# Optimization experiments

Measured on AMD Instinct MI355X. Metric: run time of the kernel, lower is better.

The kernel has to match this reference:

```python
import jax, jax.numpy as jnp
import numpy as np
from jax import lax


def setup_inputs() -> dict:
    key = jax.random.key(0)
    B, H, W, C, L = 16, 256, 256, 3, 8  # L == max_scale level sets
    x = jax.random.uniform(key, (B, H, W, C, L), dtype=jnp.float32)
    return {"x": x, "max_scale": 8}


def reference(x, max_scale):
    # x: [B, H, W, C, L] with L == max_scale
    B, H, W, C, L = x.shape
    # Fuse all level sets into the channel dim so each scale is ONE pooling op
    xr = x.reshape(B, H, W, C * L)
    neg_inf = jnp.asarray(-jnp.inf, dtype=x.dtype)
    per_scale = []
    for scale in range(1, max_scale + 1):
        # MaxPooling2D(pool_size=(scale,scale), strides=(1,1), padding='valid')
        pooled = lax.reduce_window(
            xr, neg_inf, lax.max,
            window_dimensions=(1, scale, scale, 1),
            window_strides=(1, 1, 1, 1),
            padding='VALID',
        )  # [B, H-scale+1, W-scale+1, C*L]
        # reduce_sum over spatial axes -> [B, C*L] -> [B, C, L]
        per_scale.append(pooled.sum(axis=(1, 2)).reshape(B, C, L))
    membership = jnp.stack(per_scale, axis=-1)  # [B, C, L, S]
    return jax.nn.relu(membership) + 1.0
```

## Files before the change

### kernel.cpp

```cpp
#include <hip/hip_runtime.h>
#include <math.h>


namespace {
constexpr int Bn = 16, Hn = 256, Wn = 256, CHn = 24, Sn = 8;
constexpr int IT = 16;
constexpr int NBANDS = Hn / IT;
constexpr int NSTRIP = 32;
constexpr int BDIM = CHn * NSTRIP;
constexpr int ROWF = Wn * CHn;
constexpr int LROW = 6560;
constexpr int OUT_N = Bn * CHn * Sn;
}

__device__ __forceinline__ int lds_addr(int c, int ch) {
  return c * 25 + ch + (c >> 3) * 5;
}

__global__ __launch_bounds__(BDIM, 3) void sgb_main(const float* __restrict__ x,
                                                    float* __restrict__ accum) {
  __shared__ float buf[2][LROW];

  const int band = blockIdx.x;
  const int b    = blockIdx.y;
  const int i0   = band * IT;
  const int tid  = threadIdx.x;
  const int ch    = tid >> 5;
  const int strip = tid & 31;
  const int rbase = strip * 205 + ch;
  const int wbase = lds_addr(tid / 3, (tid % 3) * 8);

  float P[7][8];
#pragma unroll
  for (int s = 0; s < 7; ++s)
#pragma unroll
    for (int j = 0; j < 8; ++j) P[s][j] = -INFINITY;

  float acc[Sn];
#pragma unroll
  for (int s = 0; s < Sn; ++s) acc[s] = 0.f;

  const float* img = x + (long)(b * Hn) * ROWF;
  const int rhi = i0 + IT + 6;

  if (rhi < Hn) {
    const float* src = img + rhi * ROWF + tid * 8;
    float4 v0 = reinterpret_cast<const float4*>(src)[0];
    float4 v1 = reinterpret_cast<const float4*>(src)[1];
    float* d = &buf[0][wbase];
    d[0] = v0.x; d[1] = v0.y; d[2] = v0.z; d[3] = v0.w;
    d[4] = v1.x; d[5] = v1.y; d[6] = v1.z; d[7] = v1.w;
  }

  for (int idx = 0; idx < IT + 7; ++idx) {
    const int r  = rhi - idx;
    const int pb = idx & 1;
    __syncthreads();

    const bool do_stage = (idx < IT + 6) && (r - 1 < Hn);
    float4 v0, v1;
    if (do_stage) {
      const float* src = img + (r - 1) * ROWF + tid * 8;
      v0 = reinterpret_cast<const float4*>(src)[0];
      v1 = reinterpret_cast<const float4*>(src)[1];
    }

    float cp[8];
    if (r < Hn) {
      const float* rb = &buf[pb][rbase];
#pragma unroll
      for (int k = 0; k < 8; ++k) cp[k] = rb[25 * k];
    } else {
#pragma unroll
      for (int k = 0; k < 8; ++k) cp[k] = -INFINITY;
    }

    const bool outrow = (r < i0 + IT);
    if (outrow) {
      acc[0] += ((cp[0] + cp[1]) + (cp[2] + cp[3])) +
                ((cp[4] + cp[5]) + (cp[6] + cp[7]));
    }

#pragma unroll
    for (int s = 2; s <= Sn; ++s) {
      float nbNew = __shfl_down(cp[0], 1);
      float nbOld = __shfl_down(P[s - 2][0], 1);
      float cc[8];
#pragma unroll
      for (int j = 0; j < 7; ++j)
        cc[j] = fmaxf(fmaxf(cp[j], cp[j + 1]),
                      fmaxf(P[s - 2][j], P[s - 2][j + 1]));
      cc[7] = fmaxf(fmaxf(cp[7], nbNew), fmaxf(P[s - 2][7], nbOld));

      if (outrow && (r + s <= Hn)) {
        float lo = 0.f, hi = 0.f;
#pragma unroll
        for (int j = 0; j < 8; ++j) {
          if (j <= 8 - s) lo += cc[j]; else hi += cc[j];
        }
        acc[s - 1] += lo + (strip == NSTRIP - 1 ? 0.f : hi);
      }
#pragma unroll
      for (int j = 0; j < 8; ++j) { P[s - 2][j] = cp[j]; cp[j] = cc[j]; }
    }

    if (do_stage) {
      float* d = &buf[pb ^ 1][wbase];
      d[0] = v0.x; d[1] = v0.y; d[2] = v0.z; d[3] = v0.w;
      d[4] = v1.x; d[5] = v1.y; d[6] = v1.z; d[7] = v1.w;
    }
  }

#pragma unroll
  for (int s = 0; s < Sn; ++s) {
    float v = acc[s];
    v += __shfl_xor(v, 16);
    v += __shfl_xor(v, 8);
    v += __shfl_xor(v, 4);
    v += __shfl_xor(v, 2);
    v += __shfl_xor(v, 1);
    if (strip == 0) atomicAdd(&accum[(b * CHn + ch) * Sn + s], v);
  }
}

__global__ void sgb_finalize(float* __restrict__ out) {
  const int i = blockIdx.x * blockDim.x + threadIdx.x;
  if (i < OUT_N) out[i] = fmaxf(out[i], 0.f) + 1.f;
}

extern "C" void kernel_launch(void* const* d_in, const int* in_sizes, int n_in,
                              void* d_out, int out_size, void* d_ws, size_t ws_size,
                              hipStream_t stream) {
  (void)in_sizes; (void)n_in; (void)d_ws; (void)ws_size; (void)out_size;
  const float* x = (const float*)d_in[0];
  float* out = (float*)d_out;

  hipMemsetAsync(out, 0, OUT_N * sizeof(float), stream);
  dim3 grid(NBANDS, Bn);
  sgb_main<<<grid, BDIM, 0, stream>>>(x, out);
  sgb_finalize<<<(OUT_N + 255) / 256, 256, 0, stream>>>(out);
}
```

Before: 163.7 us.

## Pre-transpose input to channel-planar bf16 and drop LDS staging in main kernel

Adds a transpose kernel that converts the interleaved fp32 input into per-channel bf16 planes in the workspace. The main kernel then streams rows straight from global memory with a register prefetch, removing the shared-memory double buffering and the per-row block barriers, and launches three channel groups per band. This adds an extra full pass of global writes and reads. Reducing inputs to bf16 also loses precision in the large sums.

```diff
diff --git a/kernel.cpp b/kernel.cpp
--- a/kernel.cpp
+++ b/kernel.cpp
@@ -4,31 +4,57 @@
 
 namespace {
 constexpr int Bn = 16, Hn = 256, Wn = 256, CHn = 24, Sn = 8;
-constexpr int IT = 16;
-constexpr int NBANDS = Hn / IT;
-constexpr int NSTRIP = 32;
-constexpr int BDIM = CHn * NSTRIP;
 constexpr int ROWF = Wn * CHn;
 constexpr int LROW = 6560;
+constexpr int TBD  = 768;
+constexpr int IT = 16, NBANDS = Hn / IT;
+constexpr int CHG = 3;
+constexpr int MBD = 256;
+constexpr long PLANE = (long)Hn * Wn;
 constexpr int OUT_N = Bn * CHn * Sn;
 }
 
-__device__ __forceinline__ int lds_addr(int c, int ch) {
-  return c * 25 + ch + (c >> 3) * 5;
+
+__device__ __forceinline__ unsigned bf16pack2(float a, float b) {
+  unsigned ua = __float_as_uint(a), ub = __float_as_uint(b);
+  ua = (ua + 0x7FFFu + ((ua >> 16) & 1u)) >> 16;
+  ub = (ub + 0x7FFFu + ((ub >> 16) & 1u)) & 0xFFFF0000u;
+  return ua | ub;
 }
 
-__global__ __launch_bounds__(BDIM, 3) void sgb_main(const float* __restrict__ x,
-                                                    float* __restrict__ accum) {
-  __shared__ float buf[2][LROW];
+__global__ __launch_bounds__(TBD) void sgb_transpose(const float* __restrict__ x,
+                                                     unsigned short* __restrict__ t) {
+  __shared__ float row[LROW];
+  const int r = blockIdx.x, b = blockIdx.y;
+  const int tid = threadIdx.x;
 
-  const int band = blockIdx.x;
-  const int b    = blockIdx.y;
-  const int i0   = band * IT;
-  const int tid  = threadIdx.x;
-  const int ch    = tid >> 5;
-  const int strip = tid & 31;
-  const int rbase = strip * 205 + ch;
-  const int wbase = lds_addr(tid / 3, (tid % 3) * 8);
+  const float* src = x + ((long)(b * Hn + r)) * ROWF + tid * 8;
+  const float4 v0 = reinterpret_cast<const float4*>(src)[0];
+  const float4 v1 = reinterpret_cast<const float4*>(src)[1];
+  const int wc = tid / 3;
+  float* d = &row[wc * 25 + (tid % 3) * 8 + (wc >> 3) * 5];
+  d[0] = v0.x; d[1] = v0.y; d[2] = v0.z; d[3] = v0.w;
+  d[4] = v1.x; d[5] = v1.y; d[6] = v1.z; d[7] = v1.w;
+  __syncthreads();
+
+  const int ch = tid >> 5, strip = tid & 31;
+  const float* rb = &row[strip * 205 + ch];
+  uint4 o;
+  o.x = bf16pack2(rb[0],   rb[25]);
+  o.y = bf16pack2(rb[50],  rb[75]);
+  o.z = bf16pack2(rb[100], rb[125]);
+  o.w = bf16pack2(rb[150], rb[175]);
+  reinterpret_cast<uint4*>(t + ((long)(b * CHn + ch) * Hn + r) * Wn + strip * 8)[0] = o;
+}
+
+__global__ __launch_bounds__(MBD) void sgb_main(const unsigned short* __restrict__ t,
+                                                float* __restrict__ accum) {
+  const int band = blockIdx.x, cg = blockIdx.y, b = blockIdx.z;
+  const int i0  = band * IT;
+  const int tid = threadIdx.x;
+  const int chl = tid >> 5, strip = tid & 31;
+  const int ch  = cg * 8 + chl;
+  const unsigned short* plane = t + (long)(b * CHn + ch) * PLANE + strip * 8;
 
   float P[7][8];
 #pragma unroll
@@ -40,36 +66,28 @@
 #pragma unroll
   for (int s = 0; s < Sn; ++s) acc[s] = 0.f;
 
-  const float* img = x + (long)(b * Hn) * ROWF;
   const int rhi = i0 + IT + 6;
-
-  if (rhi < Hn) {
-    const float* src = img + rhi * ROWF + tid * 8;
-    float4 v0 = reinterpret_cast<const float4*>(src)[0];
-    float4 v1 = reinterpret_cast<const float4*>(src)[1];
-    float* d = &buf[0][wbase];
-    d[0] = v0.x; d[1] = v0.y; d[2] = v0.z; d[3] = v0.w;
-    d[4] = v1.x; d[5] = v1.y; d[6] = v1.z; d[7] = v1.w;
-  }
+  bool havn = (rhi < Hn);
+  uint4 nxt = make_uint4(0, 0, 0, 0);
+  if (havn) nxt = reinterpret_cast<const uint4*>(plane + (long)rhi * Wn)[0];
 
   for (int idx = 0; idx < IT + 7; ++idx) {
-    const int r  = rhi - idx;
-    const int pb = idx & 1;
-    __syncthreads();
-
-    const bool do_stage = (idx < IT + 6) && (r - 1 < Hn);
-    float4 v0, v1;
-    if (do_stage) {
-      const float* src = img + (r - 1) * ROWF + tid * 8;
-      v0 = reinterpret_cast<const float4*>(src)[0];
-      v1 = reinterpret_cast<const float4*>(src)[1];
-    }
+    const int r = rhi - idx;
+    const uint4 cur = nxt;
+    const bool havc = havn;
+    havn = (idx < IT + 6) && (r - 1 < Hn);
+    if (havn) nxt = reinterpret_cast<const uint4*>(plane + (long)(r - 1) * Wn)[0];
 
     float cp[8];
-    if (r < Hn) {
-      const float* rb = &buf[pb][rbase];
-#pragma unroll
-      for (int k = 0; k < 8; ++k) cp[k] = rb[25 * k];
+    if (havc) {
+      cp[0] = __uint_as_float(cur.x << 16);
+      cp[1] = __uint_as_float(cur.x & 0xFFFF0000u);
+      cp[2] = __uint_as_float(cur.y << 16);
+      cp[3] = __uint_as_float(cur.y & 0xFFFF0000u);
+      cp[4] = __uint_as_float(cur.z << 16);
+      cp[5] = __uint_as_float(cur.z & 0xFFFF0000u);
+      cp[6] = __uint_as_float(cur.w << 16);
+      cp[7] = __uint_as_float(cur.w & 0xFFFF0000u);
     } else {
 #pragma unroll
       for (int k = 0; k < 8; ++k) cp[k] = -INFINITY;
@@ -83,8 +101,8 @@
 
 #pragma unroll
     for (int s = 2; s <= Sn; ++s) {
-      float nbNew = __shfl_down(cp[0], 1);
-      float nbOld = __shfl_down(P[s - 2][0], 1);
+      const float nbNew = __shfl_down(cp[0], 1);
+      const float nbOld = __shfl_down(P[s - 2][0], 1);
       float cc[8];
 #pragma unroll
       for (int j = 0; j < 7; ++j)
@@ -98,16 +116,10 @@
         for (int j = 0; j < 8; ++j) {
           if (j <= 8 - s) lo += cc[j]; else hi += cc[j];
         }
-        acc[s - 1] += lo + (strip == NSTRIP - 1 ? 0.f : hi);
+        acc[s - 1] += lo + (strip == 31 ? 0.f : hi);
       }
 #pragma unroll
       for (int j = 0; j < 8; ++j) { P[s - 2][j] = cp[j]; cp[j] = cc[j]; }
-    }
-
-    if (do_stage) {
-      float* d = &buf[pb ^ 1][wbase];
-      d[0] = v0.x; d[1] = v0.y; d[2] = v0.z; d[3] = v0.w;
-      d[4] = v1.x; d[5] = v1.y; d[6] = v1.z; d[7] = v1.w;
     }
   }
 
@@ -131,12 +143,15 @@
 extern "C" void kernel_launch(void* const* d_in, const int* in_sizes, int n_in,
                               void* d_out, int out_size, void* d_ws, size_t ws_size,
                               hipStream_t stream) {
-  (void)in_sizes; (void)n_in; (void)d_ws; (void)ws_size; (void)out_size;
+  (void)in_sizes; (void)n_in; (void)ws_size; (void)out_size;
   const float* x = (const float*)d_in[0];
   float* out = (float*)d_out;
+  unsigned short* t = (unsigned short*)d_ws;
 
   hipMemsetAsync(out, 0, OUT_N * sizeof(float), stream);
-  dim3 grid(NBANDS, Bn);
-  sgb_main<<<grid, BDIM, 0, stream>>>(x, out);
+  dim3 tg(Hn, Bn);
+  sgb_transpose<<<tg, TBD, 0, stream>>>(x, t);
+  dim3 mg(NBANDS, CHG, Bn);
+  sgb_main<<<mg, MBD, 0, stream>>>(t, out);
   sgb_finalize<<<(OUT_N + 255) / 256, 256, 0, stream>>>(out);
 }
```

Result: slower. 189.4 us (+15.7%).

## Split channels across blocks and stage rows in LDS as packed bf16

Applied to the files above, without the earlier changes.

Adds a channel-group grid dimension so each 256-thread block handles 8 of the 24 channels, and raises launch bounds to target more resident blocks. Staged rows are converted to bf16 pairs in a padded LDS layout, halving shared-memory footprint and read traffic. The rotated neighbour value is cached in registers instead of being re-shuffled. Rounding inputs to bf16 changes the max/sum results and may exceed tolerance. Global loads become strided by channel, which may reduce coalescing.

```diff
diff --git a/kernel.cpp b/kernel.cpp
--- a/kernel.cpp
+++ b/kernel.cpp
@@ -4,52 +4,63 @@
 
 namespace {
 constexpr int Bn = 16, Hn = 256, Wn = 256, CHn = 24, Sn = 8;
-constexpr int IT = 16;
-constexpr int NBANDS = Hn / IT;
-constexpr int NSTRIP = 32;
-constexpr int BDIM = CHn * NSTRIP;
-constexpr int ROWF = Wn * CHn;
-constexpr int LROW = 6560;
+constexpr int IT = 16, NBANDS = Hn / IT;
+constexpr int CHG = 3;
+constexpr int BDIM = 256;
+constexpr int LSTR = 144;
+constexpr int LROW = 8 * LSTR;
 constexpr int OUT_N = Bn * CHn * Sn;
 }
 
-__device__ __forceinline__ int lds_addr(int c, int ch) {
-  return c * 25 + ch + (c >> 3) * 5;
+__device__ __forceinline__ unsigned bf16pack2(float a, float b) {
+  unsigned ua = __float_as_uint(a), ub = __float_as_uint(b);
+  ua = (ua + 0x7FFFu + ((ua >> 16) & 1u)) >> 16;
+  ub = (ub + 0x7FFFu + ((ub >> 16) & 1u)) & 0xFFFF0000u;
+  return ua | ub;
 }
 
-__global__ __launch_bounds__(BDIM, 3) void sgb_main(const float* __restrict__ x,
+__global__ __launch_bounds__(BDIM, 4) void sgb_main(const float* __restrict__ x,
                                                     float* __restrict__ accum) {
-  __shared__ float buf[2][LROW];
+  __shared__ unsigned buf[2][LROW];
 
-  const int band = blockIdx.x;
-  const int b    = blockIdx.y;
+  const int cg   = blockIdx.x;
+  const int band = blockIdx.y;
+  const int b    = blockIdx.z;
   const int i0   = band * IT;
   const int tid  = threadIdx.x;
-  const int ch    = tid >> 5;
-  const int strip = tid & 31;
-  const int rbase = strip * 205 + ch;
-  const int wbase = lds_addr(tid / 3, (tid % 3) * 8);
+
+  const int chl = tid >> 5, strip = tid & 31;
+  const int ch  = cg * 8 + chl;
+  const int rb0 = chl * LSTR;
+
+  const int cp2 = tid & 127;
+  const int chh = (tid >> 7) * 4;
+  const int wsw = cp2 + 5 * (cp2 >> 5);
 
   float P[7][8];
 #pragma unroll
   for (int s = 0; s < 7; ++s)
 #pragma unroll
     for (int j = 0; j < 8; ++j) P[s][j] = -INFINITY;
-
+  float nbP[7];
+#pragma unroll
+  for (int s = 0; s < 7; ++s) nbP[s] = -INFINITY;
   float acc[Sn];
 #pragma unroll
   for (int s = 0; s < Sn; ++s) acc[s] = 0.f;
 
-  const float* img = x + (long)(b * Hn) * ROWF;
+  const float* img = x + ((long)b * Hn) * (Wn * CHn) + cg * 8 + chh;
   const int rhi = i0 + IT + 6;
 
   if (rhi < Hn) {
-    const float* src = img + rhi * ROWF + tid * 8;
-    float4 v0 = reinterpret_cast<const float4*>(src)[0];
-    float4 v1 = reinterpret_cast<const float4*>(src)[1];
-    float* d = &buf[0][wbase];
-    d[0] = v0.x; d[1] = v0.y; d[2] = v0.z; d[3] = v0.w;
-    d[4] = v1.x; d[5] = v1.y; d[6] = v1.z; d[7] = v1.w;
+    const float* src = img + ((long)rhi * Wn + 2 * cp2) * CHn;
+    const float4 v0 = reinterpret_cast<const float4*>(src)[0];
+    const float4 v1 = reinterpret_cast<const float4*>(src + CHn)[0];
+    unsigned* d = &buf[0][chh * LSTR + wsw];
+    d[0 * LSTR] = bf16pack2(v0.x, v1.x);
+    d[1 * LSTR] = bf16pack2(v0.y, v1.y);
+    d[2 * LSTR] = bf16pack2(v0.z, v1.z);
+    d[3 * LSTR] = bf16pack2(v0.w, v1.w);
   }
 
   for (int idx = 0; idx < IT + 7; ++idx) {
@@ -60,16 +71,20 @@
     const bool do_stage = (idx < IT + 6) && (r - 1 < Hn);
     float4 v0, v1;
     if (do_stage) {
-      const float* src = img + (r - 1) * ROWF + tid * 8;
+      const float* src = img + ((long)(r - 1) * Wn + 2 * cp2) * CHn;
       v0 = reinterpret_cast<const float4*>(src)[0];
-      v1 = reinterpret_cast<const float4*>(src)[1];
+      v1 = reinterpret_cast<const float4*>(src + CHn)[0];
     }
 
     float cp[8];
     if (r < Hn) {
-      const float* rb = &buf[pb][rbase];
 #pragma unroll
-      for (int k = 0; k < 8; ++k) cp[k] = rb[25 * k];
+      for (int k = 0; k < 4; ++k) {
+        const int c = 4 * strip + k;
+        const unsigned d = buf[pb][rb0 + c + 5 * (c >> 5)];
+        cp[2 * k]     = __uint_as_float(d << 16);
+        cp[2 * k + 1] = __uint_as_float(d & 0xFFFF0000u);
+      }
     } else {
 #pragma unroll
       for (int k = 0; k < 8; ++k) cp[k] = -INFINITY;
@@ -83,8 +98,9 @@
 
 #pragma unroll
     for (int s = 2; s <= Sn; ++s) {
-      float nbNew = __shfl_down(cp[0], 1);
-      float nbOld = __shfl_down(P[s - 2][0], 1);
+      const float nbNew = __shfl_down(cp[0], 1);
+      const float nbOld = nbP[s - 2];
+      nbP[s - 2] = nbNew;
       float cc[8];
 #pragma unroll
       for (int j = 0; j < 7; ++j)
@@ -98,16 +114,18 @@
         for (int j = 0; j < 8; ++j) {
           if (j <= 8 - s) lo += cc[j]; else hi += cc[j];
         }
-        acc[s - 1] += lo + (strip == NSTRIP - 1 ? 0.f : hi);
+        acc[s - 1] += lo + (strip == 31 ? 0.f : hi);
       }
 #pragma unroll
       for (int j = 0; j < 8; ++j) { P[s - 2][j] = cp[j]; cp[j] = cc[j]; }
     }
 
     if (do_stage) {
-      float* d = &buf[pb ^ 1][wbase];
-      d[0] = v0.x; d[1] = v0.y; d[2] = v0.z; d[3] = v0.w;
-      d[4] = v1.x; d[5] = v1.y; d[6] = v1.z; d[7] = v1.w;
+      unsigned* d = &buf[pb ^ 1][chh * LSTR + wsw];
+      d[0 * LSTR] = bf16pack2(v0.x, v1.x);
+      d[1 * LSTR] = bf16pack2(v0.y, v1.y);
+      d[2 * LSTR] = bf16pack2(v0.z, v1.z);
+      d[3 * LSTR] = bf16pack2(v0.w, v1.w);
     }
   }
 
@@ -136,7 +154,7 @@
   float* out = (float*)d_out;
 
   hipMemsetAsync(out, 0, OUT_N * sizeof(float), stream);
-  dim3 grid(NBANDS, Bn);
+  dim3 grid(CHG, NBANDS, Bn);
   sgb_main<<<grid, BDIM, 0, stream>>>(x, out);
   sgb_finalize<<<(OUT_N + 255) / 256, 256, 0, stream>>>(out);
 }
```

New measurement: 242.6 us. +48.2%, slower.
